# Kernel tuning notes

Measured on AMD Instinct MI355X. Metric: run time of the kernel, lower is better.

## Reference

```python
import jax, jax.numpy as jnp
import numpy as np

S, E, H, V = 2048, 1024, 1024, 32000


def setup_inputs() -> dict:
    key = jax.random.key(0)
    ks = jax.random.split(key, 12)
    def n(k, shape, s=0.02):
        return jax.random.normal(k, shape, dtype=jnp.float32) * s
    return {
        "encoder_out": n(ks[0], (S, E), 1.0),
        "word_input": jax.random.randint(ks[1], (1,), 0, V),
        "last_context": n(ks[2], (1, H), 1.0),
        "h0": jnp.zeros((1, 1, H), jnp.float32),
        "c0": jnp.zeros((1, 1, H), jnp.float32),
        "emb": n(ks[3], (V, E)),
        "W_ih": n(ks[4], (4 * H, E + H)),
        "b_ih": jnp.zeros((4 * H,), jnp.float32),
        "W_hh": n(ks[5], (4 * H, H)),
        "b_hh": jnp.zeros((4 * H,), jnp.float32),
        "W_att": n(ks[6], (H, E + H)),
        "b_att": jnp.zeros((H,), jnp.float32),
        "v": jax.random.uniform(ks[7], (H,), dtype=jnp.float32) * 0.1,
        "W_ah": n(ks[8], (H, E + H)),
        "b_ah": jnp.zeros((H,), jnp.float32),
        "W_out": n(ks[9], (V, H)),
        "b_out": jnp.zeros((V,), jnp.float32),
    }


def reference(encoder_out, word_input, last_context, h0, c0, emb,
              W_ih, b_ih, W_hh, b_hh, W_att, b_att, v, W_ah, b_ah,
              W_out, b_out):
    # --- single LSTM step (torch gate order: i, f, g, o) ---
    x_emb = emb[word_input[0]]                         # [E]
    lstm_in = jnp.concatenate([last_context[0], x_emb])  # [E+H]
    gates = W_ih @ lstm_in + b_ih + W_hh @ h0[0, 0] + b_hh  # [4H]
    i, f, g, o = jnp.split(gates, 4)
    i = jax.nn.sigmoid(i); f = jax.nn.sigmoid(f)
    g = jnp.tanh(g);       o = jax.nn.sigmoid(o)
    c = f * c0[0, 0] + i * g                           # [H]
    h = o * jnp.tanh(c)                                # [H] (dropout: eval = identity)

    # --- batched additive (Bahdanau-style) attention over all S steps ---
    cat = jnp.concatenate([jnp.broadcast_to(h[None, :], (S, H)), encoder_out], axis=1)  # [S, H+E]
    scores = jnp.tanh(cat @ W_att.T + b_att) @ v       # [S]
    w = jax.nn.softmax(scores)                         # [S]
    context = w @ encoder_out                          # [E]

    # --- output projection ---
    x_t = jnp.tanh(W_ah @ jnp.concatenate([context, h]) + b_ah)  # [H]
    output = jax.nn.log_softmax(W_out @ x_t + b_out)[None, :]    # [1, V]
    return (output, (h[None, None, :], c[None, None, :]), x_t[None, :], w[None, :])
```

## Files before the change

kernel.cpp:

```cpp
#include <hip/hip_runtime.h>
#include <math.h>

typedef unsigned short u16;
typedef unsigned int u32;

typedef float  floatx4 __attribute__((ext_vector_type(4)));
typedef short  shortx8 __attribute__((ext_vector_type(8)));

#define S_LEN 2048
#define E_DIM 1024
#define H_DIM 1024
#define V_DIM 32000

#define OUT_LOG 0
#define OUT_H   32000
#define OUT_C   33024
#define OUT_XT  34048
#define OUT_W   35072

#define WS_UB     0
#define WS_SCORES 1024
#define WS_CTX    3072
#define WS_MAXENC 4096
#define WS_MLZ    4097

__device__ __forceinline__ u16 f2bf(float f) {
    union { float f; u32 i; } v; v.f = f;
    u32 x = v.i;
    return (u16)((x + 0x7fffu + ((x >> 16) & 1u)) >> 16);
}
__device__ __forceinline__ u32 fenc(float f) {
    union { float f; u32 i; } v; v.f = f;
    return (v.i & 0x80000000u) ? ~v.i : (v.i | 0x80000000u);
}
__device__ __forceinline__ float fdec(u32 u) {
    union { u32 i; float f; } v;
    v.i = (u & 0x80000000u) ? (u ^ 0x80000000u) : ~u;
    return v.f;
}
__device__ __forceinline__ float wave_sum(float x) {
    #pragma unroll
    for (int m = 32; m >= 1; m >>= 1) x += __shfl_xor(x, m, 64);
    return x;
}
__device__ __forceinline__ float wave_max(float x) {
    #pragma unroll
    for (int m = 32; m >= 1; m >>= 1) x = fmaxf(x, __shfl_xor(x, m, 64));
    return x;
}

__global__ __launch_bounds__(256) void k_lstm(
    const float* __restrict__ last_ctx, const int* __restrict__ word,
    const float* __restrict__ emb, const float* __restrict__ h0,
    const float* __restrict__ c0,
    const float* __restrict__ W_ih, const float* __restrict__ b_ih,
    const float* __restrict__ W_hh, const float* __restrict__ b_hh,
    float* __restrict__ out_h, float* __restrict__ out_c)
{
    int tid = threadIdx.x;
    int w = tid >> 6, l = tid & 63;
    int j = blockIdx.x * 4 + w;

    int k0 = l * 32;
    const float* src = (l < 32) ? (last_ctx + k0)
                                : (emb + (size_t)word[0] * E_DIM + (k0 - H_DIM));
    float sv[32];
    #pragma unroll
    for (int i = 0; i < 8; ++i) *(float4*)(sv + i * 4) = *(const float4*)(src + i * 4);

    int kh = l * 16;
    float hv[16];
    #pragma unroll
    for (int i = 0; i < 4; ++i) *(float4*)(hv + i * 4) = *(const float4*)(h0 + kh + i * 4);

    float gate[4];
    #pragma unroll
    for (int gt = 0; gt < 4; ++gt) {
        int row = gt * H_DIM + j;
        const float* wrow = W_ih + (size_t)row * (E_DIM + H_DIM) + k0;
        float s = 0.f;
        #pragma unroll
        for (int i = 0; i < 8; ++i) {
            float4 wv = *(const float4*)(wrow + i * 4);
            s += wv.x * sv[i*4+0] + wv.y * sv[i*4+1] + wv.z * sv[i*4+2] + wv.w * sv[i*4+3];
        }
        const float* hrow = W_hh + (size_t)row * H_DIM + kh;
        #pragma unroll
        for (int i = 0; i < 4; ++i) {
            float4 wv = *(const float4*)(hrow + i * 4);
            s += wv.x * hv[i*4+0] + wv.y * hv[i*4+1] + wv.z * hv[i*4+2] + wv.w * hv[i*4+3];
        }
        s = wave_sum(s);
        gate[gt] = s + b_ih[row] + b_hh[row];
    }
    if (l == 0) {
        float gi = 1.f / (1.f + expf(-gate[0]));
        float gf = 1.f / (1.f + expf(-gate[1]));
        float gg = tanhf(gate[2]);
        float go = 1.f / (1.f + expf(-gate[3]));
        float c = gf * c0[j] + gi * gg;
        float h = go * tanhf(c);
        out_h[j] = h;
        out_c[j] = c;
    }
}

__global__ __launch_bounds__(256) void k_uproj(
    const float* __restrict__ W_att, const float* __restrict__ b_att,
    const float* __restrict__ out_h, float* __restrict__ wsf)
{
    int tid = threadIdx.x;
    int gid = blockIdx.x * 256 + tid;
    if (gid < S_LEN) wsf[WS_SCORES + gid] = 0.f;
    else if (gid < S_LEN + E_DIM) wsf[WS_CTX + gid - S_LEN] = 0.f;
    else if (gid == S_LEN + E_DIM) ((u32*)wsf)[WS_MAXENC] = 0u;

    int w = tid >> 6, l = tid & 63;
    int r = blockIdx.x * 4 + w;
    const float* wrow = W_att + (size_t)r * (E_DIM + H_DIM) + l * 16;
    const float* hp = out_h + l * 16;
    float s = 0.f;
    #pragma unroll
    for (int i = 0; i < 4; ++i) {
        float4 wv = *(const float4*)(wrow + i * 4);
        float4 hv = *(const float4*)(hp + i * 4);
        s += wv.x * hv.x + wv.y * hv.y + wv.z * hv.z + wv.w * hv.w;
    }
    s = wave_sum(s);
    if (l == 0) wsf[WS_UB + r] = s + b_att[r];
}

#define LDS_P 40
__global__ __launch_bounds__(256) void k_att_scores(
    const float* __restrict__ enc, const float* __restrict__ W_att,
    const float* __restrict__ vvec, const float* __restrict__ ws_ub,
    float* __restrict__ ws_scores)
{
    __shared__ u16 lds_a[64 * LDS_P];
    __shared__ u16 lds_b[128 * LDS_P];

    int tid = threadIdx.x;
    int w = tid >> 6, l = tid & 63;
    int b = blockIdx.x;
    int s0 = (b & 31) * 64;
    int r0 = (b >> 5) * 128;
    int lrow = l & 15, lq = l >> 4;

    floatx4 acc[8];
    #pragma unroll
    for (int i = 0; i < 8; ++i) acc[i] = (floatx4)0.f;

    int arow = tid >> 2, ac8 = (tid & 3) * 8;
    int brow = tid >> 1, bc16 = (tid & 1) * 16;

    for (int kc = 0; kc < 32; ++kc) {
        int e0 = kc * 32;
        __syncthreads();
        {
            const float* p = enc + (size_t)(s0 + arow) * E_DIM + e0 + ac8;
            float4 x = *(const float4*)p, y = *(const float4*)(p + 4);
            u16 tmp[8] = { f2bf(x.x), f2bf(x.y), f2bf(x.z), f2bf(x.w),
                           f2bf(y.x), f2bf(y.y), f2bf(y.z), f2bf(y.w) };
            *(uint4*)&lds_a[arow * LDS_P + ac8] = *(uint4*)tmp;
        }
        {
            const float* p = W_att + (size_t)(r0 + brow) * (E_DIM + H_DIM) + H_DIM + e0 + bc16;
            u16 tmp[16];
            #pragma unroll
            for (int m = 0; m < 16; m += 4) {
                float4 x = *(const float4*)(p + m);
                tmp[m] = f2bf(x.x); tmp[m+1] = f2bf(x.y);
                tmp[m+2] = f2bf(x.z); tmp[m+3] = f2bf(x.w);
            }
            *(uint4*)&lds_b[brow * LDS_P + bc16]     = *(uint4*)(tmp);
            *(uint4*)&lds_b[brow * LDS_P + bc16 + 8] = *(uint4*)(tmp + 8);
        }
        __syncthreads();

        shortx8 afrag = *(const shortx8*)&lds_a[(w * 16 + lrow) * LDS_P + lq * 8];
        #pragma unroll
        for (int rc = 0; rc < 8; ++rc) {
            shortx8 bfrag = *(const shortx8*)&lds_b[(rc * 16 + lrow) * LDS_P + lq * 8];
            acc[rc] = __builtin_amdgcn_mfma_f32_16x16x32_bf16(afrag, bfrag, acc[rc], 0, 0, 0);
        }
    }

    float part[4] = {0.f, 0.f, 0.f, 0.f};
    #pragma unroll
    for (int rc = 0; rc < 8; ++rc) {
        int r = r0 + rc * 16 + lrow;
        float ubr = ws_ub[r];
        float vr  = vvec[r];
        #pragma unroll
        for (int reg = 0; reg < 4; ++reg)
            part[reg] += tanhf(acc[rc][reg] + ubr) * vr;
    }
    #pragma unroll
    for (int m = 1; m < 16; m <<= 1) {
        #pragma unroll
        for (int reg = 0; reg < 4; ++reg)
            part[reg] += __shfl_xor(part[reg], m, 64);
    }
    if (lrow == 0) {
        int sbase = s0 + w * 16 + lq * 4;
        #pragma unroll
        for (int reg = 0; reg < 4; ++reg)
            atomicAdd(&ws_scores[sbase + reg], part[reg]);
    }
}

__global__ __launch_bounds__(1024) void k_softmax(
    const float* __restrict__ ws_scores, float* __restrict__ out_w)
{
    __shared__ float red[16];
    __shared__ float bmax, bsum;
    int tid = threadIdx.x;
    float s1 = ws_scores[tid], s2 = ws_scores[tid + 1024];
    float m = wave_max(fmaxf(s1, s2));
    if ((tid & 63) == 0) red[tid >> 6] = m;
    __syncthreads();
    if (tid == 0) {
        float mm = red[0];
        #pragma unroll
        for (int i = 1; i < 16; ++i) mm = fmaxf(mm, red[i]);
        bmax = mm;
    }
    __syncthreads();
    float M = bmax;
    float e1 = expf(s1 - M), e2 = expf(s2 - M);
    float s = wave_sum(e1 + e2);
    if ((tid & 63) == 0) red[tid >> 6] = s;
    __syncthreads();
    if (tid == 0) {
        float ss = 0.f;
        #pragma unroll
        for (int i = 0; i < 16; ++i) ss += red[i];
        bsum = ss;
    }
    __syncthreads();
    float inv = 1.f / bsum;
    out_w[tid] = e1 * inv; out_w[tid + 1024] = e2 * inv;
}

__global__ __launch_bounds__(256) void k_context(
    const float* __restrict__ enc, const float* __restrict__ out_w,
    float* __restrict__ ws_ctx)
{
    int tid = threadIdx.x, b = blockIdx.x;
    int e4 = tid * 4;
    int sbase = b * 32;
    float a0 = 0.f, a1 = 0.f, a2 = 0.f, a3 = 0.f;
    for (int i = 0; i < 32; ++i) {
        float wt = out_w[sbase + i];
        float4 ev = *(const float4*)(enc + (size_t)(sbase + i) * E_DIM + e4);
        a0 += wt * ev.x; a1 += wt * ev.y; a2 += wt * ev.z; a3 += wt * ev.w;
    }
    atomicAdd(&ws_ctx[e4 + 0], a0);
    atomicAdd(&ws_ctx[e4 + 1], a1);
    atomicAdd(&ws_ctx[e4 + 2], a2);
    atomicAdd(&ws_ctx[e4 + 3], a3);
}

__global__ __launch_bounds__(256) void k_xt(
    const float* __restrict__ W_ah, const float* __restrict__ b_ah,
    const float* __restrict__ ws_ctx, const float* __restrict__ out_h,
    float* __restrict__ out_xt)
{
    int tid = threadIdx.x;
    int w = tid >> 6, l = tid & 63;
    int r = blockIdx.x * 4 + w;
    int k0 = l * 32;
    const float* wrow = W_ah + (size_t)r * (E_DIM + H_DIM) + k0;
    const float* src = (l < 32) ? (ws_ctx + k0) : (out_h + (k0 - E_DIM));
    float s = 0.f;
    #pragma unroll
    for (int i = 0; i < 8; ++i) {
        float4 wv = *(const float4*)(wrow + i * 4);
        float4 sv = *(const float4*)(src + i * 4);
        s += wv.x * sv.x + wv.y * sv.y + wv.z * sv.z + wv.w * sv.w;
    }
    s = wave_sum(s);
    if (l == 0) out_xt[r] = tanhf(s + b_ah[r]);
}

__global__ __launch_bounds__(256) void k_logits(
    const float* __restrict__ W_out, const float* __restrict__ b_out,
    const float* __restrict__ out_xt,
    float* __restrict__ out_log, u32* __restrict__ ws_maxenc)
{
    __shared__ float wmax[4];
    int tid = threadIdx.x;
    int w = tid >> 6, l = tid & 63;
    int row = blockIdx.x * 4 + w;
    const float* wrow = W_out + (size_t)row * H_DIM + l * 16;
    const float* xp = out_xt + l * 16;
    float s = 0.f;
    #pragma unroll
    for (int i = 0; i < 4; ++i) {
        float4 wv = *(const float4*)(wrow + i * 4);
        float4 xv = *(const float4*)(xp + i * 4);
        s += wv.x * xv.x + wv.y * xv.y + wv.z * xv.z + wv.w * xv.w;
    }
    s = wave_sum(s);
    float lg = s + b_out[row];
    if (l == 0) { out_log[row] = lg; wmax[w] = lg; }
    __syncthreads();
    if (tid == 0) {
        float m = fmaxf(fmaxf(wmax[0], wmax[1]), fmaxf(wmax[2], wmax[3]));
        atomicMax(ws_maxenc, fenc(m));
    }
}

__global__ __launch_bounds__(1024) void k_lse(
    const float* __restrict__ out_log, const u32* __restrict__ ws_maxenc,
    float* __restrict__ ws_mlz)
{
    __shared__ float red[16];
    int tid = threadIdx.x;
    float M = fdec(ws_maxenc[0]);
    float s = 0.f;
    for (int i = tid; i < V_DIM; i += 1024) s += expf(out_log[i] - M);
    s = wave_sum(s);
    if ((tid & 63) == 0) red[tid >> 6] = s;
    __syncthreads();
    if (tid == 0) {
        float ss = 0.f;
        #pragma unroll
        for (int i = 0; i < 16; ++i) ss += red[i];
        ws_mlz[0] = M + logf(ss);
    }
}

__global__ __launch_bounds__(256) void k_writeout(
    const float* __restrict__ ws_mlz, float* __restrict__ out_log)
{
    int i = blockIdx.x * 256 + threadIdx.x;
    out_log[i] = out_log[i] - ws_mlz[0];
}

extern "C" void kernel_launch(void* const* d_in, const int* in_sizes, int n_in,
                              void* d_out, int out_size, void* d_ws, size_t ws_size,
                              hipStream_t stream) {
    const float* enc      = (const float*)d_in[0];
    const int*   word     = (const int*)d_in[1];
    const float* last_ctx = (const float*)d_in[2];
    const float* h0       = (const float*)d_in[3];
    const float* c0       = (const float*)d_in[4];
    const float* emb      = (const float*)d_in[5];
    const float* W_ih     = (const float*)d_in[6];
    const float* b_ih     = (const float*)d_in[7];
    const float* W_hh     = (const float*)d_in[8];
    const float* b_hh     = (const float*)d_in[9];
    const float* W_att    = (const float*)d_in[10];
    const float* b_att    = (const float*)d_in[11];
    const float* vvec     = (const float*)d_in[12];
    const float* W_ah     = (const float*)d_in[13];
    const float* b_ah     = (const float*)d_in[14];
    const float* W_out    = (const float*)d_in[15];
    const float* b_out    = (const float*)d_in[16];

    float* wsf = (float*)d_ws;

    float* out     = (float*)d_out;
    float* out_log = out + OUT_LOG;
    float* out_h   = out + OUT_H;
    float* out_c   = out + OUT_C;
    float* out_xt  = out + OUT_XT;
    float* out_w   = out + OUT_W;

    k_lstm<<<256, 256, 0, stream>>>(last_ctx, word, emb, h0, c0,
                                    W_ih, b_ih, W_hh, b_hh, out_h, out_c);
    k_uproj<<<256, 256, 0, stream>>>(W_att, b_att, out_h, wsf);
    k_att_scores<<<256, 256, 0, stream>>>(enc, W_att, vvec,
                                          wsf + WS_UB, wsf + WS_SCORES);
    k_softmax<<<1, 1024, 0, stream>>>(wsf + WS_SCORES, out_w);
    k_context<<<64, 256, 0, stream>>>(enc, out_w, wsf + WS_CTX);
    k_xt<<<256, 256, 0, stream>>>(W_ah, b_ah, wsf + WS_CTX, out_h, out_xt);
    k_logits<<<8000, 256, 0, stream>>>(W_out, b_out, out_xt,
                                       out_log, (u32*)wsf + WS_MAXENC);
    k_lse<<<1, 1024, 0, stream>>>(out_log, (u32*)wsf + WS_MAXENC, wsf + WS_MLZ);
    k_writeout<<<125, 256, 0, stream>>>(wsf + WS_MLZ, out_log);
}
```

Measured before the change: 443.4 us.

## Restructure GEMV kernels, enlarge attention MFMA tile, parallelize log-sum-exp

Several kernels change at once. The GEMVs in LSTM, uproj, xt and logits now assign one row per 16-lane group, with coalesced strided float4 loads and a 16-lane reduction, so fewer blocks are launched. The attention-score kernel computes a 128x128 tile per block, so each B fragment is reused across two MFMAs, and it uses a cheaper round-half-up bf16 conversion. The context kernel uses more blocks, and the single-block LSE becomes a 125-block atomic exp-sum. This cuts the serial single-block reduction and the redundant loads, at the cost of a slightly different bf16 rounding and a float atomic accumulation order.

```diff
diff --git a/kernel.cpp b/kernel.cpp
--- a/kernel.cpp
+++ b/kernel.cpp
@@ -22,12 +22,11 @@
 #define WS_SCORES 1024
 #define WS_CTX    3072
 #define WS_MAXENC 4096
-#define WS_MLZ    4097
-
-__device__ __forceinline__ u16 f2bf(float f) {
+#define WS_EXPSUM 4097
+
+__device__ __forceinline__ u16 f2bf_fast(float f) {
     union { float f; u32 i; } v; v.f = f;
-    u32 x = v.i;
-    return (u16)((x + 0x7fffu + ((x >> 16) & 1u)) >> 16);
+    return (u16)((v.i + 0x8000u) >> 16);
 }
 __device__ __forceinline__ u32 fenc(float f) {
     union { float f; u32 i; } v; v.f = f;
@@ -38,6 +37,11 @@
     v.i = (u & 0x80000000u) ? (u ^ 0x80000000u) : ~u;
     return v.f;
 }
+__device__ __forceinline__ float red16_sum(float x) {
+    #pragma unroll
+    for (int m = 1; m <= 8; m <<= 1) x += __shfl_xor(x, m, 64);
+    return x;
+}
 __device__ __forceinline__ float wave_sum(float x) {
     #pragma unroll
     for (int m = 32; m >= 1; m >>= 1) x += __shfl_xor(x, m, 64);
@@ -47,6 +51,9 @@
     #pragma unroll
     for (int m = 32; m >= 1; m >>= 1) x = fmaxf(x, __shfl_xor(x, m, 64));
     return x;
+}
+__device__ __forceinline__ float dot4(float4 a, float4 b) {
+    return a.x * b.x + a.y * b.y + a.z * b.z + a.w * b.w;
 }
 
 __global__ __launch_bounds__(256) void k_lstm(
@@ -59,45 +66,41 @@
 {
     int tid = threadIdx.x;
     int w = tid >> 6, l = tid & 63;
+    int g = l >> 4, l16 = l & 15;
     int j = blockIdx.x * 4 + w;
-
-    int k0 = l * 32;
-    const float* src = (l < 32) ? (last_ctx + k0)
-                                : (emb + (size_t)word[0] * E_DIM + (k0 - H_DIM));
-    float sv[32];
-    #pragma unroll
-    for (int i = 0; i < 8; ++i) *(float4*)(sv + i * 4) = *(const float4*)(src + i * 4);
-
-    int kh = l * 16;
-    float hv[16];
-    #pragma unroll
-    for (int i = 0; i < 4; ++i) *(float4*)(hv + i * 4) = *(const float4*)(h0 + kh + i * 4);
-
-    float gate[4];
-    #pragma unroll
-    for (int gt = 0; gt < 4; ++gt) {
-        int row = gt * H_DIM + j;
-        const float* wrow = W_ih + (size_t)row * (E_DIM + H_DIM) + k0;
-        float s = 0.f;
-        #pragma unroll
-        for (int i = 0; i < 8; ++i) {
-            float4 wv = *(const float4*)(wrow + i * 4);
-            s += wv.x * sv[i*4+0] + wv.y * sv[i*4+1] + wv.z * sv[i*4+2] + wv.w * sv[i*4+3];
-        }
-        const float* hrow = W_hh + (size_t)row * H_DIM + kh;
-        #pragma unroll
-        for (int i = 0; i < 4; ++i) {
-            float4 wv = *(const float4*)(hrow + i * 4);
-            s += wv.x * hv[i*4+0] + wv.y * hv[i*4+1] + wv.z * hv[i*4+2] + wv.w * hv[i*4+3];
-        }
-        s = wave_sum(s);
-        gate[gt] = s + b_ih[row] + b_hh[row];
-    }
+    int row = g * H_DIM + j;
+    const float* embrow = emb + (size_t)word[0] * E_DIM;
+    const float* wrow = W_ih + (size_t)row * (E_DIM + H_DIM);
+    const float* hrow = W_hh + (size_t)row * H_DIM;
+    int c4 = l16 * 4;
+
+    float s = 0.f;
+    #pragma unroll 4
+    for (int it = 0; it < 16; ++it) {
+        int col = it * 64 + c4;
+        s += dot4(*(const float4*)(wrow + col), *(const float4*)(last_ctx + col));
+    }
+    #pragma unroll 4
+    for (int it = 0; it < 16; ++it) {
+        int col = it * 64 + c4;
+        s += dot4(*(const float4*)(wrow + 1024 + col), *(const float4*)(embrow + col));
+    }
+    #pragma unroll 4
+    for (int it = 0; it < 16; ++it) {
+        int col = it * 64 + c4;
+        s += dot4(*(const float4*)(hrow + col), *(const float4*)(h0 + col));
+    }
+    s = red16_sum(s);
+    if (l16 == 0) s += b_ih[row] + b_hh[row];
+    float g0 = __shfl(s, 0,  64);
+    float g1 = __shfl(s, 16, 64);
+    float g2 = __shfl(s, 32, 64);
+    float g3 = __shfl(s, 48, 64);
     if (l == 0) {
-        float gi = 1.f / (1.f + expf(-gate[0]));
-        float gf = 1.f / (1.f + expf(-gate[1]));
-        float gg = tanhf(gate[2]);
-        float go = 1.f / (1.f + expf(-gate[3]));
+        float gi = 1.f / (1.f + expf(-g0));
+        float gf = 1.f / (1.f + expf(-g1));
+        float gg = tanhf(g2);
+        float go = 1.f / (1.f + expf(-g3));
         float c = gf * c0[j] + gi * gg;
         float h = go * tanhf(c);
         out_h[j] = h;
@@ -114,20 +117,21 @@
     if (gid < S_LEN) wsf[WS_SCORES + gid] = 0.f;
     else if (gid < S_LEN + E_DIM) wsf[WS_CTX + gid - S_LEN] = 0.f;
     else if (gid == S_LEN + E_DIM) ((u32*)wsf)[WS_MAXENC] = 0u;
+    else if (gid == S_LEN + E_DIM + 1) wsf[WS_EXPSUM] = 0.f;
 
     int w = tid >> 6, l = tid & 63;
-    int r = blockIdx.x * 4 + w;
-    const float* wrow = W_att + (size_t)r * (E_DIM + H_DIM) + l * 16;
-    const float* hp = out_h + l * 16;
+    int sub = l >> 4, l16 = l & 15;
+    int r = blockIdx.x * 16 + w * 4 + sub;
+    const float* wrow = W_att + (size_t)r * (E_DIM + H_DIM);
+    int c4 = l16 * 4;
     float s = 0.f;
-    #pragma unroll
-    for (int i = 0; i < 4; ++i) {
-        float4 wv = *(const float4*)(wrow + i * 4);
-        float4 hv = *(const float4*)(hp + i * 4);
-        s += wv.x * hv.x + wv.y * hv.y + wv.z * hv.z + wv.w * hv.w;
-    }
-    s = wave_sum(s);
-    if (l == 0) wsf[WS_UB + r] = s + b_att[r];
+    #pragma unroll 4
+    for (int it = 0; it < 16; ++it) {
+        int col = it * 64 + c4;
+        s += dot4(*(const float4*)(wrow + col), *(const float4*)(out_h + col));
+    }
+    s = red16_sum(s);
+    if (l16 == 0) wsf[WS_UB + r] = s + b_att[r];
 }
 
 #define LDS_P 40
@@ -136,76 +140,91 @@
     const float* __restrict__ vvec, const float* __restrict__ ws_ub,
     float* __restrict__ ws_scores)
 {
-    __shared__ u16 lds_a[64 * LDS_P];
+    __shared__ u16 lds_a[128 * LDS_P];
     __shared__ u16 lds_b[128 * LDS_P];
 
     int tid = threadIdx.x;
     int w = tid >> 6, l = tid & 63;
     int b = blockIdx.x;
-    int s0 = (b & 31) * 64;
-    int r0 = (b >> 5) * 128;
+    int s0 = (b & 15) * 128;
+    int r0 = (b >> 4) * 128;
     int lrow = l & 15, lq = l >> 4;
 
-    floatx4 acc[8];
-    #pragma unroll
-    for (int i = 0; i < 8; ++i) acc[i] = (floatx4)0.f;
-
-    int arow = tid >> 2, ac8 = (tid & 3) * 8;
-    int brow = tid >> 1, bc16 = (tid & 1) * 16;
+    floatx4 acc[2][8];
+    #pragma unroll
+    for (int sf = 0; sf < 2; ++sf)
+        #pragma unroll
+        for (int i = 0; i < 8; ++i) acc[sf][i] = (floatx4)0.f;
+
+    int srow = tid >> 1, scol = (tid & 1) * 16;
 
     for (int kc = 0; kc < 32; ++kc) {
         int e0 = kc * 32;
         __syncthreads();
         {
-            const float* p = enc + (size_t)(s0 + arow) * E_DIM + e0 + ac8;
-            float4 x = *(const float4*)p, y = *(const float4*)(p + 4);
-            u16 tmp[8] = { f2bf(x.x), f2bf(x.y), f2bf(x.z), f2bf(x.w),
-                           f2bf(y.x), f2bf(y.y), f2bf(y.z), f2bf(y.w) };
-            *(uint4*)&lds_a[arow * LDS_P + ac8] = *(uint4*)tmp;
-        }
-        {
-            const float* p = W_att + (size_t)(r0 + brow) * (E_DIM + H_DIM) + H_DIM + e0 + bc16;
+            const float* p = enc + (size_t)(s0 + srow) * E_DIM + e0 + scol;
             u16 tmp[16];
             #pragma unroll
             for (int m = 0; m < 16; m += 4) {
                 float4 x = *(const float4*)(p + m);
-                tmp[m] = f2bf(x.x); tmp[m+1] = f2bf(x.y);
-                tmp[m+2] = f2bf(x.z); tmp[m+3] = f2bf(x.w);
+                tmp[m] = f2bf_fast(x.x); tmp[m+1] = f2bf_fast(x.y);
+                tmp[m+2] = f2bf_fast(x.z); tmp[m+3] = f2bf_fast(x.w);
             }
-            *(uint4*)&lds_b[brow * LDS_P + bc16]     = *(uint4*)(tmp);
-            *(uint4*)&lds_b[brow * LDS_P + bc16 + 8] = *(uint4*)(tmp + 8);
+            *(uint4*)&lds_a[srow * LDS_P + scol]     = *(uint4*)(tmp);
+            *(uint4*)&lds_a[srow * LDS_P + scol + 8] = *(uint4*)(tmp + 8);
+        }
+        {
+            const float* p = W_att + (size_t)(r0 + srow) * (E_DIM + H_DIM) + H_DIM + e0 + scol;
+            u16 tmp[16];
+            #pragma unroll
+            for (int m = 0; m < 16; m += 4) {
+                float4 x = *(const float4*)(p + m);
+                tmp[m] = f2bf_fast(x.x); tmp[m+1] = f2bf_fast(x.y);
+                tmp[m+2] = f2bf_fast(x.z); tmp[m+3] = f2bf_fast(x.w);
+            }
+            *(uint4*)&lds_b[srow * LDS_P + scol]     = *(uint4*)(tmp);
+            *(uint4*)&lds_b[srow * LDS_P + scol + 8] = *(uint4*)(tmp + 8);
         }
         __syncthreads();
 
-        shortx8 afrag = *(const shortx8*)&lds_a[(w * 16 + lrow) * LDS_P + lq * 8];
+        shortx8 afrag[2];
+        afrag[0] = *(const shortx8*)&lds_a[(w * 32 + lrow) * LDS_P + lq * 8];
+        afrag[1] = *(const shortx8*)&lds_a[(w * 32 + 16 + lrow) * LDS_P + lq * 8];
         #pragma unroll
         for (int rc = 0; rc < 8; ++rc) {
             shortx8 bfrag = *(const shortx8*)&lds_b[(rc * 16 + lrow) * LDS_P + lq * 8];
-            acc[rc] = __builtin_amdgcn_mfma_f32_16x16x32_bf16(afrag, bfrag, acc[rc], 0, 0, 0);
+            acc[0][rc] = __builtin_amdgcn_mfma_f32_16x16x32_bf16(afrag[0], bfrag, acc[0][rc], 0, 0, 0);
+            acc[1][rc] = __builtin_amdgcn_mfma_f32_16x16x32_bf16(afrag[1], bfrag, acc[1][rc], 0, 0, 0);
         }
     }
 
-    float part[4] = {0.f, 0.f, 0.f, 0.f};
+    float part[2][4] = {{0.f,0.f,0.f,0.f},{0.f,0.f,0.f,0.f}};
     #pragma unroll
     for (int rc = 0; rc < 8; ++rc) {
         int r = r0 + rc * 16 + lrow;
         float ubr = ws_ub[r];
         float vr  = vvec[r];
         #pragma unroll
-        for (int reg = 0; reg < 4; ++reg)
-            part[reg] += tanhf(acc[rc][reg] + ubr) * vr;
-    }
-    #pragma unroll
-    for (int m = 1; m < 16; m <<= 1) {
-        #pragma unroll
-        for (int reg = 0; reg < 4; ++reg)
-            part[reg] += __shfl_xor(part[reg], m, 64);
-    }
+        for (int sf = 0; sf < 2; ++sf)
+            #pragma unroll
+            for (int reg = 0; reg < 4; ++reg)
+                part[sf][reg] += tanhf(acc[sf][rc][reg] + ubr) * vr;
+    }
+    #pragma unroll
+    for (int m = 1; m <= 8; m <<= 1)
+        #pragma unroll
+        for (int sf = 0; sf < 2; ++sf)
+            #pragma unroll
+            for (int reg = 0; reg < 4; ++reg)
+                part[sf][reg] += __shfl_xor(part[sf][reg], m, 64);
     if (lrow == 0) {
-        int sbase = s0 + w * 16 + lq * 4;
-        #pragma unroll
-        for (int reg = 0; reg < 4; ++reg)
-            atomicAdd(&ws_scores[sbase + reg], part[reg]);
+        #pragma unroll
+        for (int sf = 0; sf < 2; ++sf) {
+            int sbase = s0 + w * 32 + sf * 16 + lq * 4;
+            #pragma unroll
+            for (int reg = 0; reg < 4; ++reg)
+                atomicAdd(&ws_scores[sbase + reg], part[sf][reg]);
+        }
     }
 }
 
@@ -248,9 +267,10 @@
 {
     int tid = threadIdx.x, b = blockIdx.x;
     int e4 = tid * 4;
-    int sbase = b * 32;
+    int sbase = b * 16;
     float a0 = 0.f, a1 = 0.f, a2 = 0.f, a3 = 0.f;
-    for (int i = 0; i < 32; ++i) {
+    #pragma unroll 4
+    for (int i = 0; i < 16; ++i) {
         float wt = out_w[sbase + i];
         float4 ev = *(const float4*)(enc + (size_t)(sbase + i) * E_DIM + e4);
         a0 += wt * ev.x; a1 += wt * ev.y; a2 += wt * ev.z; a3 += wt * ev.w;
@@ -268,19 +288,23 @@
 {
     int tid = threadIdx.x;
     int w = tid >> 6, l = tid & 63;
-    int r = blockIdx.x * 4 + w;
-    int k0 = l * 32;
-    const float* wrow = W_ah + (size_t)r * (E_DIM + H_DIM) + k0;
-    const float* src = (l < 32) ? (ws_ctx + k0) : (out_h + (k0 - E_DIM));
+    int sub = l >> 4, l16 = l & 15;
+    int r = blockIdx.x * 16 + w * 4 + sub;
+    const float* wrow = W_ah + (size_t)r * (E_DIM + H_DIM);
+    int c4 = l16 * 4;
     float s = 0.f;
-    #pragma unroll
-    for (int i = 0; i < 8; ++i) {
-        float4 wv = *(const float4*)(wrow + i * 4);
-        float4 sv = *(const float4*)(src + i * 4);
-        s += wv.x * sv.x + wv.y * sv.y + wv.z * sv.z + wv.w * sv.w;
-    }
-    s = wave_sum(s);
-    if (l == 0) out_xt[r] = tanhf(s + b_ah[r]);
+    #pragma unroll 4
+    for (int it = 0; it < 16; ++it) {
+        int col = it * 64 + c4;
+        s += dot4(*(const float4*)(wrow + col), *(const float4*)(ws_ctx + col));
+    }
+    #pragma unroll 4
+    for (int it = 0; it < 16; ++it) {
+        int col = it * 64 + c4;
+        s += dot4(*(const float4*)(wrow + 1024 + col), *(const float4*)(out_h + col));
+    }
+    s = red16_sum(s);
+    if (l16 == 0) out_xt[r] = tanhf(s + b_ah[r]);
 }
 
 __global__ __launch_bounds__(256) void k_logits(
@@ -291,19 +315,22 @@
     __shared__ float wmax[4];
     int tid = threadIdx.x;
     int w = tid >> 6, l = tid & 63;
-    int row = blockIdx.x * 4 + w;
-    const float* wrow = W_out + (size_t)row * H_DIM + l * 16;
-    const float* xp = out_xt + l * 16;
+    int sub = l >> 4, l16 = l & 15;
+    int row = blockIdx.x * 16 + w * 4 + sub;
+    const float* wrow = W_out + (size_t)row * H_DIM;
+    int c4 = l16 * 4;
     float s = 0.f;
-    #pragma unroll
-    for (int i = 0; i < 4; ++i) {
-        float4 wv = *(const float4*)(wrow + i * 4);
-        float4 xv = *(const float4*)(xp + i * 4);
-        s += wv.x * xv.x + wv.y * xv.y + wv.z * xv.z + wv.w * xv.w;
-    }
-    s = wave_sum(s);
+    #pragma unroll 4
+    for (int it = 0; it < 16; ++it) {
+        int col = it * 64 + c4;
+        s += dot4(*(const float4*)(wrow + col), *(const float4*)(out_xt + col));
+    }
+    s = red16_sum(s);
     float lg = s + b_out[row];
-    if (l == 0) { out_log[row] = lg; wmax[w] = lg; }
+    float wm = -1e30f;
+    if (l16 == 0) { out_log[row] = lg; wm = lg; }
+    wm = wave_max(wm);
+    if (l == 0) wmax[w] = wm;
     __syncthreads();
     if (tid == 0) {
         float m = fmaxf(fmaxf(wmax[0], wmax[1]), fmaxf(wmax[2], wmax[3]));
@@ -311,31 +338,29 @@
     }
 }
 
-__global__ __launch_bounds__(1024) void k_lse(
+__global__ __launch_bounds__(256) void k_lse(
     const float* __restrict__ out_log, const u32* __restrict__ ws_maxenc,
-    float* __restrict__ ws_mlz)
-{
-    __shared__ float red[16];
-    int tid = threadIdx.x;
+    float* __restrict__ ws_expsum)
+{
+    __shared__ float red[4];
+    int tid = threadIdx.x;
+    int i = blockIdx.x * 256 + tid;
     float M = fdec(ws_maxenc[0]);
-    float s = 0.f;
-    for (int i = tid; i < V_DIM; i += 1024) s += expf(out_log[i] - M);
+    float s = expf(out_log[i] - M);
     s = wave_sum(s);
     if ((tid & 63) == 0) red[tid >> 6] = s;
     __syncthreads();
-    if (tid == 0) {
-        float ss = 0.f;
-        #pragma unroll
-        for (int i = 0; i < 16; ++i) ss += red[i];
-        ws_mlz[0] = M + logf(ss);
-    }
+    if (tid == 0)
+        atomicAdd(ws_expsum, red[0] + red[1] + red[2] + red[3]);
 }
 
 __global__ __launch_bounds__(256) void k_writeout(
-    const float* __restrict__ ws_mlz, float* __restrict__ out_log)
+    const u32* __restrict__ ws_maxenc, const float* __restrict__ ws_expsum,
+    float* __restrict__ out_log)
 {
     int i = blockIdx.x * 256 + threadIdx.x;
-    out_log[i] = out_log[i] - ws_mlz[0];
+    float lz = fdec(ws_maxenc[0]) + logf(ws_expsum[0]);
+    out_log[i] = out_log[i] - lz;
 }
 
 extern "C" void kernel_launch(void* const* d_in, const int* in_sizes, int n_in,
@@ -370,14 +395,16 @@
 
     k_lstm<<<256, 256, 0, stream>>>(last_ctx, word, emb, h0, c0,
                                     W_ih, b_ih, W_hh, b_hh, out_h, out_c);
-    k_uproj<<<256, 256, 0, stream>>>(W_att, b_att, out_h, wsf);
-    k_att_scores<<<256, 256, 0, stream>>>(enc, W_att, vvec,
+    k_uproj<<<64, 256, 0, stream>>>(W_att, b_att, out_h, wsf);
+    k_att_scores<<<128, 256, 0, stream>>>(enc, W_att, vvec,
                                           wsf + WS_UB, wsf + WS_SCORES);
     k_softmax<<<1, 1024, 0, stream>>>(wsf + WS_SCORES, out_w);
-    k_context<<<64, 256, 0, stream>>>(enc, out_w, wsf + WS_CTX);
-    k_xt<<<256, 256, 0, stream>>>(W_ah, b_ah, wsf + WS_CTX, out_h, out_xt);
-    k_logits<<<8000, 256, 0, stream>>>(W_out, b_out, out_xt,
+    k_context<<<128, 256, 0, stream>>>(enc, out_w, wsf + WS_CTX);
+    k_xt<<<64, 256, 0, stream>>>(W_ah, b_ah, wsf + WS_CTX, out_h, out_xt);
+    k_logits<<<2000, 256, 0, stream>>>(W_out, b_out, out_xt,
                                        out_log, (u32*)wsf + WS_MAXENC);
-    k_lse<<<1, 1024, 0, stream>>>(out_log, (u32*)wsf + WS_MAXENC, wsf + WS_MLZ);
-    k_writeout<<<125, 256, 0, stream>>>(wsf + WS_MLZ, out_log);
-}
+    k_lse<<<125, 256, 0, stream>>>(out_log, (u32*)wsf + WS_MAXENC,
+                                   wsf + WS_EXPSUM);
+    k_writeout<<<125, 256, 0, stream>>>((u32*)wsf + WS_MAXENC,
+                                        wsf + WS_EXPSUM, out_log);
+}
```

Measured after the change: 401.4 us. -9.5%, faster.
